# Optimization experiments

Measured on AMD Instinct MI355X. Metric: run time of the kernel, lower is better.

Reference implementation:

```python
import jax, jax.numpy as jnp
import numpy as np

B, H, N, Dh = 4, 16, 8192, 64
EPS = 1e-5          # masked-fill epsilon for D
CLAMP_EPS = 1e-10   # clamp_abs epsilon for gamma denominator
PROJ_EPS = 4e-3     # geoopt float32 projection epsilon


def _sumsq(x):
    return jnp.sum(x * x, axis=-1, keepdims=True)


def _pt0back(x, v, k):
    # geoopt parallel_transport0back: transport v from x back to origin
    # = v * lambda_x / lambda_0 = v / (1 + k ||x||^2)
    return v / jnp.maximum(1.0 + k * _sumsq(x), 1e-15)


def _lambda_x(x, k):
    # conformal factor 2 / (1 + k ||x||^2)
    return 2.0 / jnp.maximum(1.0 + k * _sumsq(x), 1e-15)


def _clamp_abs(x, eps):
    s = jnp.where(x >= 0, 1.0, -1.0)
    return s * jnp.maximum(jnp.abs(x), eps)


def _project(x, k):
    # clip points to the ball of radius (1-eps)/sqrt(|k|) when k < 0
    maxnorm = jnp.where(k < 0, (1.0 - PROJ_EPS) / jnp.sqrt(jnp.abs(k) + 1e-15), 1e15)
    norm = jnp.maximum(jnp.linalg.norm(x, axis=-1, keepdims=True), 1e-15)
    return jnp.where(norm > maxnorm, x / norm * maxnorm, x)


def _artan_k(u, k):
    sk = jnp.sqrt(jnp.abs(k) + 1e-15)
    su = sk * u
    hyp = jnp.arctanh(jnp.clip(su, -1.0 + 1e-7, 1.0 - 1e-7))
    return jnp.where(k < 0, hyp, jnp.arctan(su)) / sk


def _tan_k(u, k):
    sk = jnp.sqrt(jnp.abs(k) + 1e-15)
    su = sk * u
    return jnp.where(k < 0, jnp.tanh(su), jnp.tan(su)) / sk


def _mobius_scalar_mul(r, x, k):
    xnorm = jnp.maximum(jnp.linalg.norm(x, axis=-1, keepdims=True), 1e-15)
    return _tan_k(r * _artan_k(xnorm, k), k) * x / xnorm


def setup_inputs() -> dict:
    key = jax.random.key(0)
    kq, kk, kv = jax.random.split(key, 3)
    Q = 0.5 * jax.random.normal(kq, (B, H, N, Dh), dtype=jnp.float32)
    K = 0.5 * jax.random.normal(kk, (B, H, N, Dh), dtype=jnp.float32)
    # scale V so points lie well inside the Poincare ball: ||V||^2 ~ 0.16 < 1/|k|
    V = 0.05 * jax.random.normal(kv, (B, H, N, Dh), dtype=jnp.float32)
    mask = jnp.ones((N,), dtype=jnp.float32)
    curvatures = jnp.linspace(-2.0, -0.5, H, dtype=jnp.float32).reshape(H, 1, 1)
    return {"Q": Q, "K": K, "V": V, "mask": mask, "curvatures": curvatures}


def reference(Q, K, V, mask, curvatures):
    k = curvatures                      # [H,1,1], broadcasts over [B,H,N,1]
    m = mask[None, :, None]             # [1,N,1] -> broadcasts over [B,H,N,D]
    v1 = _pt0back(V, Q, k)              # transport Q from V back to origin
    v2 = _pt0back(V, K, k)
    gamma = _lambda_x(V, k)             # [B,H,N,1]
    denom = _clamp_abs(gamma - 1.0, CLAMP_EPS)
    x = gamma / denom * V * m           # [B,H,N,D]
    v1 = jax.nn.elu(v1) + 1.0           # positive feature map
    v2 = denom * (jax.nn.elu(v2) + 1.0) * m
    v2_sum = jnp.sum(v2, axis=-2)       # [B,H,D]
    Dn = jnp.einsum('bhnd,bhd->bhn', v1, v2_sum)
    D_inv = 1.0 / jnp.where(Dn == 0, EPS, Dn)
    context = jnp.einsum('bhnd,bhne->bhde', v2, x)          # [B,H,D,D]
    X = jnp.einsum('bhde,bhnd,bhn->bhne', context, v1, D_inv)
    X = _project(X, k)
    X = _mobius_scalar_mul(0.5, X, k)
    X = _project(X, k)
    return X
```

## Files before the change

### kernel.cpp

```cpp
#include <hip/hip_runtime.h>
#include <math.h>

#define NROWS   8192
#define DHH     64
#define BHCOUNT 64
#define HCOUNT  16
#define SPLITA  16
#define CHUNKA  (NROWS / SPLITA)
#define GA      32
#define LSTR    68
#define SPLITB  32
#define CHUNKB  (NROWS / SPLITB)
#define CTXSZ   4160
#define EPS_DN  1e-5f
#define PROJ_EPS 0.004f

__device__ __forceinline__ float elu1(float x) {
    return x > 0.0f ? x + 1.0f : expf(x);
}

__global__ __launch_bounds__(256) void phaseA(
        const float* __restrict__ Kp, const float* __restrict__ Vp,
        const float* __restrict__ maskp, const float* __restrict__ curvp,
        float* __restrict__ denomWs, float* __restrict__ partials) {
    __shared__ __align__(16) float smem[2 * GA * LSTR];
    float* v2s = smem;
    float* xs  = smem + GA * LSTR;

    const int bx = blockIdx.x;
    const int bh = bx / SPLITA, sp = bx % SPLITA;
    const float k = curvp[bh % HCOUNT];
    const int t = threadIdx.x;
    const int rowBase = sp * CHUNKA;
    const float* Kb = Kp + (size_t)bh * NROWS * DHH;
    const float* Vb = Vp + (size_t)bh * NROWS * DHH;

    const int wave = t >> 6;
    const int lane = t & 63;
    const int d0 = (lane >> 3) * 8;
    const int e0 = (lane & 7) * 8;
    const int rloc = t >> 4;
    const int c4   = t & 15;

    float acc[8][8];
    #pragma unroll
    for (int i = 0; i < 8; ++i)
        #pragma unroll
        for (int j = 0; j < 8; ++j) acc[i][j] = 0.f;
    float4 v2sum4 = make_float4(0.f, 0.f, 0.f, 0.f);

    for (int g = 0; g < CHUNKA / GA; ++g) {
        #pragma unroll
        for (int pass = 0; pass < 2; ++pass) {
            const int rl = pass * 16 + rloc;
            const int n = rowBase + g * GA + rl;
            const float4 v4 = *(const float4*)(Vb + (size_t)n * DHH + 4 * c4);
            const float4 k4 = *(const float4*)(Kb + (size_t)n * DHH + 4 * c4);
            float ss = v4.x*v4.x + v4.y*v4.y + v4.z*v4.z + v4.w*v4.w;
            ss += __shfl_xor(ss, 1);
            ss += __shfl_xor(ss, 2);
            ss += __shfl_xor(ss, 4);
            ss += __shfl_xor(ss, 8);
            const float dv    = fmaxf(1.0f + k * ss, 1e-15f);
            const float gamma = 2.0f / dv;
            const float gm1   = gamma - 1.0f;
            const float dnm   = (gm1 >= 0.0f ? 1.0f : -1.0f) * fmaxf(fabsf(gm1), 1e-10f);
            const float m     = maskp[n];
            const float idv   = 1.0f / dv;
            const float cv2   = dnm * m;
            const float cx    = (gamma / dnm) * m;
            float4 v2v, xv;
            v2v.x = cv2 * elu1(k4.x * idv);
            v2v.y = cv2 * elu1(k4.y * idv);
            v2v.z = cv2 * elu1(k4.z * idv);
            v2v.w = cv2 * elu1(k4.w * idv);
            xv.x = cx * v4.x; xv.y = cx * v4.y; xv.z = cx * v4.z; xv.w = cx * v4.w;
            *(float4*)&v2s[rl * LSTR + 4 * c4] = v2v;
            *(float4*)&xs [rl * LSTR + 4 * c4] = xv;
            v2sum4.x += v2v.x; v2sum4.y += v2v.y; v2sum4.z += v2v.z; v2sum4.w += v2v.w;
            if (c4 == 0) denomWs[(size_t)bh * NROWS + n] = dv;
        }
        __syncthreads();
        #pragma unroll 2
        for (int r = wave; r < GA; r += 4) {
            const float4 alo = *(const float4*)&v2s[r * LSTR + d0];
            const float4 ahi = *(const float4*)&v2s[r * LSTR + d0 + 4];
            const float4 blo = *(const float4*)&xs [r * LSTR + e0];
            const float4 bhi = *(const float4*)&xs [r * LSTR + e0 + 4];
            const float af[8] = {alo.x, alo.y, alo.z, alo.w, ahi.x, ahi.y, ahi.z, ahi.w};
            const float bf[8] = {blo.x, blo.y, blo.z, blo.w, bhi.x, bhi.y, bhi.z, bhi.w};
            #pragma unroll
            for (int i = 0; i < 8; ++i)
                #pragma unroll
                for (int j = 0; j < 8; ++j)
                    acc[i][j] += af[i] * bf[j];
        }
        __syncthreads();
    }

    float* red = smem;
    for (int w = 0; w < 4; ++w) {
        if (wave == w) {
            #pragma unroll
            for (int i = 0; i < 8; ++i) {
                const int base = (d0 + i) * DHH + e0;
                float4 lo = make_float4(acc[i][0], acc[i][1], acc[i][2], acc[i][3]);
                float4 hi = make_float4(acc[i][4], acc[i][5], acc[i][6], acc[i][7]);
                if (w != 0) {
                    const float4 plo = *(const float4*)&red[base];
                    const float4 phi = *(const float4*)&red[base + 4];
                    lo.x += plo.x; lo.y += plo.y; lo.z += plo.z; lo.w += plo.w;
                    hi.x += phi.x; hi.y += phi.y; hi.z += phi.z; hi.w += phi.w;
                }
                *(float4*)&red[base]     = lo;
                *(float4*)&red[base + 4] = hi;
            }
        }
        __syncthreads();
    }

    float* pbase = partials + (size_t)(bh * SPLITA + sp) * CTXSZ;
    #pragma unroll
    for (int i = 0; i < 4; ++i) {
        const int idx = t * 16 + i * 4;
        *(float4*)(pbase + idx) = *(const float4*)&red[idx];
    }
    __syncthreads();
    *(float4*)&smem[t * 4] = v2sum4;
    __syncthreads();
    if (t < DHH) {
        const int cc = t >> 2, j = t & 3;
        float s = 0.f;
        #pragma unroll
        for (int q = 0; q < 16; ++q) s += smem[(q * 16 + cc) * 4 + j];
        pbase[4096 + t] = s;
    }
}

__global__ __launch_bounds__(256) void reduceCtx(
        const float* __restrict__ partials, float* __restrict__ ctxsum) {
    const int bh = blockIdx.x;
    const int t = threadIdx.x;
    for (int idx = t; idx < CTXSZ; idx += 256) {
        const float* p = partials + (size_t)bh * SPLITA * CTXSZ + idx;
        float s = 0.f;
        #pragma unroll
        for (int sp = 0; sp < SPLITA; ++sp) s += p[(size_t)sp * CTXSZ];
        ctxsum[(size_t)bh * CTXSZ + idx] = s;
    }
}

__global__ __launch_bounds__(256) void phaseB(
        const float* __restrict__ Qp, const float* __restrict__ curvp,
        const float* __restrict__ denomWs, const float* __restrict__ ctxsum,
        float* __restrict__ outp) {
    __shared__ __align__(16) float ctx[DHH * LSTR];
    __shared__ __align__(16) float v1s[64 * LSTR];
    __shared__ __align__(16) float v2sum[DHH];
    __shared__ float dinv[64];
    __shared__ float rowsq[64 * 17];
    __shared__ float factor[64];

    const int bx = blockIdx.x;
    const int bh = bx / SPLITB, sp = bx % SPLITB;
    const float k = curvp[bh % HCOUNT];
    const float sk = sqrtf(fabsf(k) + 1e-15f);
    const float maxnorm = (k < 0.0f) ? (1.0f - PROJ_EPS) / sk : 1e15f;
    const int t = threadIdx.x;

    const float* cb = ctxsum + (size_t)bh * CTXSZ;
    #pragma unroll
    for (int i = 0; i < 16; ++i) {
        const int idx = i * 256 + t;
        ctx[(idx >> 6) * LSTR + (idx & 63)] = cb[idx];
    }
    if (t < DHH) v2sum[t] = cb[4096 + t];
    __syncthreads();

    const float* Qb  = Qp  + (size_t)bh * NROWS * DHH;
    float*       Ob  = outp + (size_t)bh * NROWS * DHH;
    const float* dvb = denomWs + (size_t)bh * NROWS;
    const int rloc = t >> 4, c4 = t & 15;
    const int tr = t >> 4, tc = t & 15;

    for (int tile = 0; tile < CHUNKB / 64; ++tile) {
        const int n0 = sp * CHUNKB + tile * 64;
        #pragma unroll
        for (int pass = 0; pass < 4; ++pass) {
            const int rl = pass * 16 + rloc;
            const int n = n0 + rl;
            const float4 q4 = *(const float4*)(Qb + (size_t)n * DHH + 4 * c4);
            const float dv = dvb[n];
            const float idv = 1.0f / dv;
            float4 v14;
            v14.x = elu1(q4.x * idv);
            v14.y = elu1(q4.y * idv);
            v14.z = elu1(q4.z * idv);
            v14.w = elu1(q4.w * idv);
            *(float4*)&v1s[rl * LSTR + 4 * c4] = v14;
            const float4 vs = *(const float4*)&v2sum[4 * c4];
            float dn = v14.x * vs.x + v14.y * vs.y + v14.z * vs.z + v14.w * vs.w;
            dn += __shfl_xor(dn, 1);
            dn += __shfl_xor(dn, 2);
            dn += __shfl_xor(dn, 4);
            dn += __shfl_xor(dn, 8);
            if (c4 == 0) {
                const float Dd = (dn == 0.0f) ? EPS_DN : dn;
                dinv[rl] = 1.0f / Dd;
            }
        }
        __syncthreads();
        float acc[4][4] = {{0.f,0.f,0.f,0.f},{0.f,0.f,0.f,0.f},{0.f,0.f,0.f,0.f},{0.f,0.f,0.f,0.f}};
        #pragma unroll 2
        for (int d0 = 0; d0 < DHH; d0 += 4) {
            float4 cv[4], av[4];
            #pragma unroll
            for (int q = 0; q < 4; ++q) cv[q] = *(const float4*)&ctx[(d0 + q) * LSTR + 4 * tc];
            #pragma unroll
            for (int i = 0; i < 4; ++i) av[i] = *(const float4*)&v1s[(4 * tr + i) * LSTR + d0];
            #pragma unroll
            for (int i = 0; i < 4; ++i) {
                acc[i][0] += av[i].x*cv[0].x + av[i].y*cv[1].x + av[i].z*cv[2].x + av[i].w*cv[3].x;
                acc[i][1] += av[i].x*cv[0].y + av[i].y*cv[1].y + av[i].z*cv[2].y + av[i].w*cv[3].y;
                acc[i][2] += av[i].x*cv[0].z + av[i].y*cv[1].z + av[i].z*cv[2].z + av[i].w*cv[3].z;
                acc[i][3] += av[i].x*cv[0].w + av[i].y*cv[1].w + av[i].z*cv[2].w + av[i].w*cv[3].w;
            }
        }
        #pragma unroll
        for (int i = 0; i < 4; ++i) {
            const float di = dinv[4 * tr + i];
            acc[i][0] *= di; acc[i][1] *= di; acc[i][2] *= di; acc[i][3] *= di;
            const float ps = acc[i][0]*acc[i][0] + acc[i][1]*acc[i][1]
                           + acc[i][2]*acc[i][2] + acc[i][3]*acc[i][3];
            rowsq[(4 * tr + i) * 17 + tc] = ps;
        }
        __syncthreads();
        if (t < 64) {
            float s = 0.f;
            #pragma unroll
            for (int q = 0; q < 16; ++q) s += rowsq[t * 17 + q];
            const float norm = fmaxf(sqrtf(s), 1e-15f);
            const float f1 = (norm > maxnorm) ? (maxnorm / norm) : 1.0f;
            const float n2 = norm * f1;
            const float xnorm = fmaxf(n2, 1e-15f);
            const float su = sk * xnorm;
            const float suc = fminf(su, 1.0f - 1e-7f);
            float tk;
            if (k < 0.0f) tk = tanhf(0.5f * atanhf(suc));
            else          tk = tanf(0.5f * atanf(su));
            tk = tk / sk;
            const float f2 = tk / xnorm;
            const float n3 = fmaxf(fabsf(tk), 1e-15f);
            const float f3 = (n3 > maxnorm) ? (maxnorm / n3) : 1.0f;
            factor[t] = f1 * f2 * f3;
        }
        __syncthreads();
        #pragma unroll
        for (int i = 0; i < 4; ++i) {
            const float f = factor[4 * tr + i];
            float4 o = make_float4(acc[i][0] * f, acc[i][1] * f, acc[i][2] * f, acc[i][3] * f);
            *(float4*)(Ob + (size_t)(n0 + 4 * tr + i) * DHH + 4 * tc) = o;
        }
        __syncthreads();
    }
}

extern "C" void kernel_launch(void* const* d_in, const int* in_sizes, int n_in,
                              void* d_out, int out_size, void* d_ws, size_t ws_size,
                              hipStream_t stream) {
    const float* Q    = (const float*)d_in[0];
    const float* K    = (const float*)d_in[1];
    const float* V    = (const float*)d_in[2];
    const float* mask = (const float*)d_in[3];
    const float* curv = (const float*)d_in[4];
    float* out = (float*)d_out;

    float* denomWs  = (float*)d_ws;
    float* partials = denomWs + (size_t)BHCOUNT * NROWS;
    float* ctxsum   = partials + (size_t)BHCOUNT * SPLITA * CTXSZ;

    phaseA<<<dim3(BHCOUNT * SPLITA), dim3(256), 0, stream>>>(K, V, mask, curv, denomWs, partials);
    reduceCtx<<<dim3(BHCOUNT), dim3(256), 0, stream>>>(partials, ctxsum);
    phaseB<<<dim3(BHCOUNT * SPLITB), dim3(256), 0, stream>>>(Q, curv, denomWs, ctxsum, out);
}
```

Measured before the change: 476.9 us.

## Prefetch and double-buffer phaseA, split reduce, rewrite phaseB with register-resident context

phaseA now prefetches the next K/V tile into registers and double-buffers shared memory, which removes one barrier per group. reduceCtx is split into 16 segments per head so more blocks run in parallel. phaseB is rewritten so each wave handles 64 rows: the context matrix lives in registers, v1 is broadcast through readlane, Q is loaded one row at a time with prefetch, and tanh(0.5*atanh) is replaced by a closed-form algebraic identity. Together these aim to cut shared-memory traffic, barriers and transcendental calls. The cost is heavy register pressure in phaseB (a 64-float context array plus launch bounds asking for 4 blocks), and the per-row readlane loop may be slower than the old tiled matmul.

```diff
diff --git a/kernel.cpp b/kernel.cpp
--- a/kernel.cpp
+++ b/kernel.cpp
@@ -14,19 +14,21 @@
 #define CTXSZ   4160
 #define EPS_DN  1e-5f
 #define PROJ_EPS 0.004f
+#define NGA     (CHUNKA / GA)
+#define ABUF    (2 * GA * LSTR)
 
 __device__ __forceinline__ float elu1(float x) {
     return x > 0.0f ? x + 1.0f : expf(x);
 }
-
-__global__ __launch_bounds__(256) void phaseA(
+__device__ __forceinline__ float rlane(float v, int l) {
+    return __uint_as_float(__builtin_amdgcn_readlane(__float_as_uint(v), l));
+}
+
+__global__ __launch_bounds__(256, 4) void phaseA(
         const float* __restrict__ Kp, const float* __restrict__ Vp,
         const float* __restrict__ maskp, const float* __restrict__ curvp,
         float* __restrict__ denomWs, float* __restrict__ partials) {
-    __shared__ __align__(16) float smem[2 * GA * LSTR];
-    float* v2s = smem;
-    float* xs  = smem + GA * LSTR;
-
+    __shared__ __align__(16) float smem[2 * ABUF];
     const int bx = blockIdx.x;
     const int bh = bx / SPLITA, sp = bx % SPLITA;
     const float k = curvp[bh % HCOUNT];
@@ -49,13 +51,32 @@
         for (int j = 0; j < 8; ++j) acc[i][j] = 0.f;
     float4 v2sum4 = make_float4(0.f, 0.f, 0.f, 0.f);
 
-    for (int g = 0; g < CHUNKA / GA; ++g) {
+    float4 pV[2], pK[2];
+    #pragma unroll
+    for (int pass = 0; pass < 2; ++pass) {
+        const int n = rowBase + pass * 16 + rloc;
+        pV[pass] = *(const float4*)(Vb + (size_t)n * DHH + 4 * c4);
+        pK[pass] = *(const float4*)(Kb + (size_t)n * DHH + 4 * c4);
+    }
+
+    for (int g = 0; g < NGA; ++g) {
+        float4 nV[2], nK[2];
+        if (g + 1 < NGA) {
+            #pragma unroll
+            for (int pass = 0; pass < 2; ++pass) {
+                const int n = rowBase + (g + 1) * GA + pass * 16 + rloc;
+                nV[pass] = *(const float4*)(Vb + (size_t)n * DHH + 4 * c4);
+                nK[pass] = *(const float4*)(Kb + (size_t)n * DHH + 4 * c4);
+            }
+        }
+        float* v2s = smem + (g & 1) * ABUF;
+        float* xs  = v2s + GA * LSTR;
         #pragma unroll
         for (int pass = 0; pass < 2; ++pass) {
             const int rl = pass * 16 + rloc;
             const int n = rowBase + g * GA + rl;
-            const float4 v4 = *(const float4*)(Vb + (size_t)n * DHH + 4 * c4);
-            const float4 k4 = *(const float4*)(Kb + (size_t)n * DHH + 4 * c4);
+            const float4 v4 = pV[pass];
+            const float4 k4 = pK[pass];
             float ss = v4.x*v4.x + v4.y*v4.y + v4.z*v4.z + v4.w*v4.w;
             ss += __shfl_xor(ss, 1);
             ss += __shfl_xor(ss, 2);
@@ -95,8 +116,9 @@
                 for (int j = 0; j < 8; ++j)
                     acc[i][j] += af[i] * bf[j];
         }
-        __syncthreads();
-    }
+        pV[0] = nV[0]; pV[1] = nV[1]; pK[0] = nK[0]; pK[1] = nK[1];
+    }
+    __syncthreads();
 
     float* red = smem;
     for (int w = 0; w < 4; ++w) {
@@ -137,11 +159,15 @@
     }
 }
 
+#define RSEG 16
 __global__ __launch_bounds__(256) void reduceCtx(
         const float* __restrict__ partials, float* __restrict__ ctxsum) {
-    const int bh = blockIdx.x;
+    const int bh  = blockIdx.x / RSEG;
+    const int seg = blockIdx.x % RSEG;
     const int t = threadIdx.x;
-    for (int idx = t; idx < CTXSZ; idx += 256) {
+    const int base = seg * 260;
+    for (int i = t; i < 260; i += 256) {
+        const int idx = base + i;
         const float* p = partials + (size_t)bh * SPLITA * CTXSZ + idx;
         float s = 0.f;
         #pragma unroll
@@ -150,118 +176,105 @@
     }
 }
 
-__global__ __launch_bounds__(256) void phaseB(
+__global__ __launch_bounds__(256, 4) void phaseB(
         const float* __restrict__ Qp, const float* __restrict__ curvp,
         const float* __restrict__ denomWs, const float* __restrict__ ctxsum,
         float* __restrict__ outp) {
-    __shared__ __align__(16) float ctx[DHH * LSTR];
-    __shared__ __align__(16) float v1s[64 * LSTR];
-    __shared__ __align__(16) float v2sum[DHH];
-    __shared__ float dinv[64];
-    __shared__ float rowsq[64 * 17];
-    __shared__ float factor[64];
-
     const int bx = blockIdx.x;
     const int bh = bx / SPLITB, sp = bx % SPLITB;
     const float k = curvp[bh % HCOUNT];
     const float sk = sqrtf(fabsf(k) + 1e-15f);
     const float maxnorm = (k < 0.0f) ? (1.0f - PROJ_EPS) / sk : 1e15f;
     const int t = threadIdx.x;
+    const int wave = t >> 6;
+    const int lane = t & 63;
 
     const float* cb = ctxsum + (size_t)bh * CTXSZ;
-    #pragma unroll
-    for (int i = 0; i < 16; ++i) {
-        const int idx = i * 256 + t;
-        ctx[(idx >> 6) * LSTR + (idx & 63)] = cb[idx];
-    }
-    if (t < DHH) v2sum[t] = cb[4096 + t];
-    __syncthreads();
-
-    const float* Qb  = Qp  + (size_t)bh * NROWS * DHH;
+    float ctxr[DHH];
+    #pragma unroll
+    for (int d = 0; d < DHH; ++d) ctxr[d] = cb[d * DHH + lane];
+    const float v2s = cb[4096 + lane];
+
+    const float* Qb  = Qp   + (size_t)bh * NROWS * DHH;
     float*       Ob  = outp + (size_t)bh * NROWS * DHH;
     const float* dvb = denomWs + (size_t)bh * NROWS;
-    const int rloc = t >> 4, c4 = t & 15;
-    const int tr = t >> 4, tc = t & 15;
-
-    for (int tile = 0; tile < CHUNKB / 64; ++tile) {
-        const int n0 = sp * CHUNKB + tile * 64;
-        #pragma unroll
-        for (int pass = 0; pass < 4; ++pass) {
-            const int rl = pass * 16 + rloc;
-            const int n = n0 + rl;
-            const float4 q4 = *(const float4*)(Qb + (size_t)n * DHH + 4 * c4);
-            const float dv = dvb[n];
-            const float idv = 1.0f / dv;
-            float4 v14;
-            v14.x = elu1(q4.x * idv);
-            v14.y = elu1(q4.y * idv);
-            v14.z = elu1(q4.z * idv);
-            v14.w = elu1(q4.w * idv);
-            *(float4*)&v1s[rl * LSTR + 4 * c4] = v14;
-            const float4 vs = *(const float4*)&v2sum[4 * c4];
-            float dn = v14.x * vs.x + v14.y * vs.y + v14.z * vs.z + v14.w * vs.w;
-            dn += __shfl_xor(dn, 1);
-            dn += __shfl_xor(dn, 2);
-            dn += __shfl_xor(dn, 4);
-            dn += __shfl_xor(dn, 8);
-            if (c4 == 0) {
-                const float Dd = (dn == 0.0f) ? EPS_DN : dn;
-                dinv[rl] = 1.0f / Dd;
-            }
-        }
-        __syncthreads();
-        float acc[4][4] = {{0.f,0.f,0.f,0.f},{0.f,0.f,0.f,0.f},{0.f,0.f,0.f,0.f},{0.f,0.f,0.f,0.f}};
-        #pragma unroll 2
-        for (int d0 = 0; d0 < DHH; d0 += 4) {
-            float4 cv[4], av[4];
-            #pragma unroll
-            for (int q = 0; q < 4; ++q) cv[q] = *(const float4*)&ctx[(d0 + q) * LSTR + 4 * tc];
-            #pragma unroll
-            for (int i = 0; i < 4; ++i) av[i] = *(const float4*)&v1s[(4 * tr + i) * LSTR + d0];
-            #pragma unroll
-            for (int i = 0; i < 4; ++i) {
-                acc[i][0] += av[i].x*cv[0].x + av[i].y*cv[1].x + av[i].z*cv[2].x + av[i].w*cv[3].x;
-                acc[i][1] += av[i].x*cv[0].y + av[i].y*cv[1].y + av[i].z*cv[2].y + av[i].w*cv[3].y;
-                acc[i][2] += av[i].x*cv[0].z + av[i].y*cv[1].z + av[i].z*cv[2].z + av[i].w*cv[3].z;
-                acc[i][3] += av[i].x*cv[0].w + av[i].y*cv[1].w + av[i].z*cv[2].w + av[i].w*cv[3].w;
-            }
-        }
-        #pragma unroll
-        for (int i = 0; i < 4; ++i) {
-            const float di = dinv[4 * tr + i];
-            acc[i][0] *= di; acc[i][1] *= di; acc[i][2] *= di; acc[i][3] *= di;
-            const float ps = acc[i][0]*acc[i][0] + acc[i][1]*acc[i][1]
-                           + acc[i][2]*acc[i][2] + acc[i][3]*acc[i][3];
-            rowsq[(4 * tr + i) * 17 + tc] = ps;
-        }
-        __syncthreads();
-        if (t < 64) {
-            float s = 0.f;
-            #pragma unroll
-            for (int q = 0; q < 16; ++q) s += rowsq[t * 17 + q];
-            const float norm = fmaxf(sqrtf(s), 1e-15f);
-            const float f1 = (norm > maxnorm) ? (maxnorm / norm) : 1.0f;
-            const float n2 = norm * f1;
-            const float xnorm = fmaxf(n2, 1e-15f);
-            const float su = sk * xnorm;
+    const int n0 = sp * CHUNKB + wave * 64;
+    const int lm = lane & 3;
+
+    float qc0 = Qb[(size_t)(n0 + 0) * DHH + lane];
+    float qc1 = Qb[(size_t)(n0 + 1) * DHH + lane];
+    float qc2 = Qb[(size_t)(n0 + 2) * DHH + lane];
+    float qc3 = Qb[(size_t)(n0 + 3) * DHH + lane];
+    float dc0 = dvb[n0 + 0], dc1 = dvb[n0 + 1], dc2 = dvb[n0 + 2], dc3 = dvb[n0 + 3];
+
+    #pragma unroll 1
+    for (int g = 0; g < 16; ++g) {
+        const int nb = n0 + g * 4;
+        float qn0, qn1, qn2, qn3, dn0, dn1, dn2, dn3;
+        if (g < 15) {
+            qn0 = Qb[(size_t)(nb + 4) * DHH + lane];
+            qn1 = Qb[(size_t)(nb + 5) * DHH + lane];
+            qn2 = Qb[(size_t)(nb + 6) * DHH + lane];
+            qn3 = Qb[(size_t)(nb + 7) * DHH + lane];
+            dn0 = dvb[nb + 4]; dn1 = dvb[nb + 5]; dn2 = dvb[nb + 6]; dn3 = dvb[nb + 7];
+        }
+        const float v10 = elu1(qc0 * (1.0f / dc0));
+        const float v11 = elu1(qc1 * (1.0f / dc1));
+        const float v12 = elu1(qc2 * (1.0f / dc2));
+        const float v13 = elu1(qc3 * (1.0f / dc3));
+        float t0 = v10 * v2s, t1 = v11 * v2s, t2 = v12 * v2s, t3 = v13 * v2s;
+        t0 += __shfl_xor(t0, 1); t1 += __shfl_xor(t1, 1);
+        t2 += __shfl_xor(t2, 1); t3 += __shfl_xor(t3, 1);
+        t0 += __shfl_xor(t0, 2); t1 += __shfl_xor(t1, 2);
+        t2 += __shfl_xor(t2, 2); t3 += __shfl_xor(t3, 2);
+        float p = (lm == 0) ? t0 : (lm == 1) ? t1 : (lm == 2) ? t2 : t3;
+        p += __shfl_xor(p, 4); p += __shfl_xor(p, 8);
+        p += __shfl_xor(p, 16); p += __shfl_xor(p, 32);
+        p = (p == 0.0f) ? EPS_DN : p;
+        const float pinv = 1.0f / p;
+        const float di0 = rlane(pinv, 0), di1 = rlane(pinv, 1);
+        const float di2 = rlane(pinv, 2), di3 = rlane(pinv, 3);
+        float a0 = 0.f, a1 = 0.f, a2 = 0.f, a3 = 0.f;
+        #pragma unroll
+        for (int d = 0; d < DHH; ++d) {
+            a0 = fmaf(rlane(v10, d), ctxr[d], a0);
+            a1 = fmaf(rlane(v11, d), ctxr[d], a1);
+            a2 = fmaf(rlane(v12, d), ctxr[d], a2);
+            a3 = fmaf(rlane(v13, d), ctxr[d], a3);
+        }
+        a0 *= di0; a1 *= di1; a2 *= di2; a3 *= di3;
+        float u0 = a0 * a0, u1 = a1 * a1, u2 = a2 * a2, u3 = a3 * a3;
+        u0 += __shfl_xor(u0, 1); u1 += __shfl_xor(u1, 1);
+        u2 += __shfl_xor(u2, 1); u3 += __shfl_xor(u3, 1);
+        u0 += __shfl_xor(u0, 2); u1 += __shfl_xor(u1, 2);
+        u2 += __shfl_xor(u2, 2); u3 += __shfl_xor(u3, 2);
+        float s = (lm == 0) ? u0 : (lm == 1) ? u1 : (lm == 2) ? u2 : u3;
+        s += __shfl_xor(s, 4); s += __shfl_xor(s, 8);
+        s += __shfl_xor(s, 16); s += __shfl_xor(s, 32);
+        const float norm = fmaxf(sqrtf(s), 1e-15f);
+        const float f1 = (norm > maxnorm) ? (maxnorm / norm) : 1.0f;
+        const float xnorm = fmaxf(norm * f1, 1e-15f);
+        const float su = sk * xnorm;
+        float tk;
+        if (k < 0.0f) {
             const float suc = fminf(su, 1.0f - 1e-7f);
-            float tk;
-            if (k < 0.0f) tk = tanhf(0.5f * atanhf(suc));
-            else          tk = tanf(0.5f * atanf(su));
-            tk = tk / sk;
-            const float f2 = tk / xnorm;
-            const float n3 = fmaxf(fabsf(tk), 1e-15f);
-            const float f3 = (n3 > maxnorm) ? (maxnorm / n3) : 1.0f;
-            factor[t] = f1 * f2 * f3;
-        }
-        __syncthreads();
-        #pragma unroll
-        for (int i = 0; i < 4; ++i) {
-            const float f = factor[4 * tr + i];
-            float4 o = make_float4(acc[i][0] * f, acc[i][1] * f, acc[i][2] * f, acc[i][3] * f);
-            *(float4*)(Ob + (size_t)(n0 + 4 * tr + i) * DHH + 4 * tc) = o;
-        }
-        __syncthreads();
+            tk = suc / (1.0f + sqrtf(fmaxf(1.0f - suc * suc, 0.0f)));
+        } else {
+            tk = su / (1.0f + sqrtf(1.0f + su * su));
+        }
+        tk /= sk;
+        const float f2 = tk / xnorm;
+        const float n3 = fmaxf(fabsf(tk), 1e-15f);
+        const float f3 = (n3 > maxnorm) ? (maxnorm / n3) : 1.0f;
+        const float fac = f1 * f2 * f3;
+        const float f0_ = rlane(fac, 0), f1_ = rlane(fac, 1);
+        const float f2_ = rlane(fac, 2), f3_ = rlane(fac, 3);
+        Ob[(size_t)(nb + 0) * DHH + lane] = a0 * f0_;
+        Ob[(size_t)(nb + 1) * DHH + lane] = a1 * f1_;
+        Ob[(size_t)(nb + 2) * DHH + lane] = a2 * f2_;
+        Ob[(size_t)(nb + 3) * DHH + lane] = a3 * f3_;
+        qc0 = qn0; qc1 = qn1; qc2 = qn2; qc3 = qn3;
+        dc0 = dn0; dc1 = dn1; dc2 = dn2; dc3 = dn3;
     }
 }
 
@@ -280,6 +293,6 @@
     float* ctxsum   = partials + (size_t)BHCOUNT * SPLITA * CTXSZ;
 
     phaseA<<<dim3(BHCOUNT * SPLITA), dim3(256), 0, stream>>>(K, V, mask, curv, denomWs, partials);
-    reduceCtx<<<dim3(BHCOUNT), dim3(256), 0, stream>>>(partials, ctxsum);
+    reduceCtx<<<dim3(BHCOUNT * RSEG), dim3(256), 0, stream>>>(partials, ctxsum);
     phaseB<<<dim3(BHCOUNT * SPLITB), dim3(256), 0, stream>>>(Q, curv, denomWs, ctxsum, out);
 }
```

After: 578.2 us. 21.2% more time.
